# Kernel tuning notes

Measured on AMD Instinct MI355X. Metric: run time of the kernel, lower is better.

## Reference

```python
import jax, jax.numpy as jnp
import numpy as np

K = 2  # top-k experts per token


def setup_inputs() -> dict:
    key = jax.random.key(0)
    k1, k2 = jax.random.split(key)
    B, S, H, E = 4, 4096, 4096, 64
    x = jax.random.normal(k1, (B, S, H), dtype=jnp.float32)
    gate_w = jax.random.normal(k2, (E, H), dtype=jnp.float32) * (H ** -0.5)
    return {"x": x, "gate_w": gate_w}


def reference(x, gate_w):
    # logits = x @ gate_w.T : [B, S, E]
    logits = jnp.einsum("bsh,eh->bse", x, gate_w)
    scores = jax.nn.softmax(logits, axis=-1)
    topk_scores, topk_idx = jax.lax.top_k(scores, K)  # [B, S, K]
    aux_loss = scores.mean() * 0.0
    z_loss = jnp.mean(logits.astype(jnp.float32) ** 2)
    return topk_idx, topk_scores, aux_loss, z_loss
```

## Files before the change

kernel.cpp:

```cpp
#include <hip/hip_runtime.h>
#include <hip/hip_bf16.h>


typedef __bf16  bf16x8  __attribute__((ext_vector_type(8)));
typedef float   f32x16  __attribute__((ext_vector_type(16)));

#define BS_TOK 16384
#define H_DIM  4096
#define E_DIM  64
#define KSPLIT 4
#define KCHUNK (H_DIM / KSPLIT)
#define NPANEL (KCHUNK / 64)
#define WS_ZBUF_OFF (1536u << 10)
#define WS_LG_OFF   (2u << 20)

__device__ __forceinline__ void split3(float v, __bf16 &b0, __bf16 &b1, __bf16 &b2) {
    b0 = (__bf16)v;
    float r = v - (float)b0;
    b1 = (__bf16)r;
    float r2 = r - (float)b1;
    b2 = (__bf16)r2;
}

__device__ __forceinline__ void async_copy16(const float* gp, float* lp) {
    __builtin_amdgcn_global_load_lds(
        (const __attribute__((address_space(1))) void*)gp,
        (__attribute__((address_space(3))) void*)lp, 16, 0, 0);
}

__global__ void prep_w(const float* __restrict__ gw, bf16x8* __restrict__ wb) {
    int idx  = blockIdx.x * blockDim.x + threadIdx.x;
    int kb   = idx >> 7;
    int rem  = idx & 127;
    int nt   = rem >> 6;
    int lane = rem & 63;
    int n  = nt * 32 + (lane & 31);
    int kk = kb * 16 + ((lane >> 5) << 3);
    const float* p = gw + (size_t)n * H_DIM + kk;
    bf16x8 t0, t1, t2;
#pragma unroll
    for (int j = 0; j < 8; ++j) {
        __bf16 a, b, c;
        split3(p[j], a, b, c);
        t0[j] = a; t1[j] = b; t2[j] = c;
    }
    size_t fb = (size_t)(kb * 2 + nt) * 3;
    wb[(fb + 0) * 64 + lane] = t0;
    wb[(fb + 1) * 64 + lane] = t1;
    wb[(fb + 2) * 64 + lane] = t2;
}

__global__ __launch_bounds__(256, 4) void gemm_split(
        const float* __restrict__ x, const bf16x8* __restrict__ wb,
        float* __restrict__ lg) {
    __shared__ float lds[2 * 4096];

    int bid = blockIdx.x;
    int mt  = bid >> 2;
    int kc  = bid & 3;
    int tid = threadIdx.x;
    int w   = tid >> 6;
    int l   = tid & 63;
    int m0  = mt * 64;
    int rw  = (w & 1) * 32;
    int kh  = w >> 1;

    const float* gpan[4];
    int ldso[4];
    int s_slot = l & 15;
#pragma unroll
    for (int r = 0; r < 4; ++r) {
        int g = r * 16 + w * 4 + (l >> 4);
        int c = s_slot ^ (g & 15);
        gpan[r] = x + (size_t)(m0 + g) * H_DIM + kc * KCHUNK + c * 4;
        ldso[r] = (r * 16 + w * 4) * 64;
    }

    f32x16 acc0, acc1;
#pragma unroll
    for (int r = 0; r < 16; ++r) { acc0[r] = 0.f; acc1[r] = 0.f; }

#pragma unroll
    for (int r = 0; r < 4; ++r) async_copy16(gpan[r], &lds[ldso[r]]);

    int row  = rw + (l & 31);
    int half = l >> 5;
    int rsw  = row & 15;

    for (int p = 0; p < NPANEL; ++p) {
        __syncthreads();
        if (p + 1 < NPANEL) {
            int b = (p + 1) & 1;
#pragma unroll
            for (int r = 0; r < 4; ++r)
                async_copy16(gpan[r] + (p + 1) * 64, &lds[b * 4096 + ldso[r]]);
        }
        int bufo = (p & 1) * 4096;
#pragma unroll
        for (int ks2 = 0; ks2 < 2; ++ks2) {
            int ks     = kh * 2 + ks2;
            int ks_abs = kc * 64 + p * 4 + ks;
            int c0     = ks * 4 + half * 2;
            float4 xa = *(const float4*)&lds[bufo + row * 64 + ((c0 ^ rsw) << 2)];
            float4 xb = *(const float4*)&lds[bufo + row * 64 + (((c0 + 1) ^ rsw) << 2)];
            bf16x8 a0, a1, a2;
            float xs[8] = {xa.x, xa.y, xa.z, xa.w, xb.x, xb.y, xb.z, xb.w};
#pragma unroll
            for (int j = 0; j < 8; ++j) {
                __bf16 h0, h1, h2;
                split3(xs[j], h0, h1, h2);
                a0[j] = h0; a1[j] = h1; a2[j] = h2;
            }
            const bf16x8* wp = wb + (size_t)ks_abs * 6 * 64 + l;
            bf16x8 b0 = wp[0*64], b1 = wp[1*64], b2 = wp[2*64];
            bf16x8 b3 = wp[3*64], b4 = wp[4*64], b5 = wp[5*64];
            acc0 = __builtin_amdgcn_mfma_f32_32x32x16_bf16(a0, b0, acc0, 0, 0, 0);
            acc0 = __builtin_amdgcn_mfma_f32_32x32x16_bf16(a1, b0, acc0, 0, 0, 0);
            acc0 = __builtin_amdgcn_mfma_f32_32x32x16_bf16(a2, b0, acc0, 0, 0, 0);
            acc0 = __builtin_amdgcn_mfma_f32_32x32x16_bf16(a0, b1, acc0, 0, 0, 0);
            acc0 = __builtin_amdgcn_mfma_f32_32x32x16_bf16(a1, b1, acc0, 0, 0, 0);
            acc0 = __builtin_amdgcn_mfma_f32_32x32x16_bf16(a0, b2, acc0, 0, 0, 0);
            acc1 = __builtin_amdgcn_mfma_f32_32x32x16_bf16(a0, b3, acc1, 0, 0, 0);
            acc1 = __builtin_amdgcn_mfma_f32_32x32x16_bf16(a1, b3, acc1, 0, 0, 0);
            acc1 = __builtin_amdgcn_mfma_f32_32x32x16_bf16(a2, b3, acc1, 0, 0, 0);
            acc1 = __builtin_amdgcn_mfma_f32_32x32x16_bf16(a0, b4, acc1, 0, 0, 0);
            acc1 = __builtin_amdgcn_mfma_f32_32x32x16_bf16(a1, b4, acc1, 0, 0, 0);
            acc1 = __builtin_amdgcn_mfma_f32_32x32x16_bf16(a0, b5, acc1, 0, 0, 0);
        }
    }

    int col = l & 31;
    if (kh == 1) {
#pragma unroll
        for (int r = 0; r < 16; ++r) {
            int mm = rw + (r & 3) + ((r >> 2) << 3) + (half << 2);
            lds[mm * 64 + col]      = acc0[r];
            lds[mm * 64 + 32 + col] = acc1[r];
        }
    }
    __syncthreads();
    if (kh == 0) {
        size_t obase = (size_t)kc * BS_TOK * E_DIM + (size_t)m0 * E_DIM;
#pragma unroll
        for (int r = 0; r < 16; ++r) {
            int mm = rw + (r & 3) + ((r >> 2) << 3) + (half << 2);
            lg[obase + (size_t)mm * E_DIM + col]
                = acc0[r] + lds[mm * 64 + col];
            lg[obase + (size_t)mm * E_DIM + 32 + col]
                = acc1[r] + lds[mm * 64 + 32 + col];
        }
    }
}

__global__ __launch_bounds__(256) void epilogue(const float* __restrict__ lg,
                                                float* __restrict__ out,
                                                float* __restrict__ zbuf) {
    __shared__ float zsh[4];
    int lane = threadIdx.x & 63;
    int w    = threadIdx.x >> 6;
    int t    = blockIdx.x * 4 + w;

    float l = 0.f;
#pragma unroll
    for (int s = 0; s < KSPLIT; ++s)
        l += lg[((size_t)s * BS_TOK + t) * E_DIM + lane];

    float z = l * l;
#pragma unroll
    for (int off = 32; off; off >>= 1) z += __shfl_xor(z, off);
    if (lane == 0) zsh[w] = z;

    float m = l;
#pragma unroll
    for (int off = 32; off; off >>= 1) m = fmaxf(m, __shfl_xor(m, off));
    float e = expf(l - m);
    float d = e;
#pragma unroll
    for (int off = 32; off; off >>= 1) d += __shfl_xor(d, off);
    float sc = e / d;

    float s1 = sc; int i1 = lane;
#pragma unroll
    for (int off = 32; off; off >>= 1) {
        float os = __shfl_xor(s1, off); int oi = __shfl_xor(i1, off);
        if (os > s1 || (os == s1 && oi < i1)) { s1 = os; i1 = oi; }
    }
    float sm = (lane == i1) ? -1.0f : sc;
    float s2 = sm; int i2 = lane;
#pragma unroll
    for (int off = 32; off; off >>= 1) {
        float os = __shfl_xor(s2, off); int oi = __shfl_xor(i2, off);
        if (os > s2 || (os == s2 && oi < i2)) { s2 = os; i2 = oi; }
    }

    if (lane == 0) {
        out[2 * t]                  = (float)i1;
        out[2 * t + 1]              = (float)i2;
        out[2 * BS_TOK + 2 * t]     = s1;
        out[2 * BS_TOK + 2 * t + 1] = s2;
    }
    __syncthreads();
    if (threadIdx.x == 0)
        zbuf[blockIdx.x] = zsh[0] + zsh[1] + zsh[2] + zsh[3];
}

__global__ __launch_bounds__(256) void zreduce(const float* __restrict__ zbuf,
                                               float* __restrict__ out) {
    __shared__ float sh[4];
    int tid = threadIdx.x;
    float s = 0.f;
#pragma unroll
    for (int i = 0; i < 16; ++i) s += zbuf[tid + 256 * i];
#pragma unroll
    for (int off = 32; off; off >>= 1) s += __shfl_xor(s, off);
    if ((tid & 63) == 0) sh[tid >> 6] = s;
    __syncthreads();
    if (tid == 0) {
        out[4 * BS_TOK]     = 0.0f;
        out[4 * BS_TOK + 1] = (sh[0] + sh[1] + sh[2] + sh[3])
                              * (1.0f / (float)(BS_TOK * E_DIM));
    }
}

extern "C" void kernel_launch(void* const* d_in, const int* in_sizes, int n_in,
                              void* d_out, int out_size, void* d_ws, size_t ws_size,
                              hipStream_t stream) {
    const float* x  = (const float*)d_in[0];
    const float* gw = (const float*)d_in[1];
    float* out  = (float*)d_out;
    bf16x8* wb  = (bf16x8*)d_ws;
    float*  zbf = (float*)((char*)d_ws + WS_ZBUF_OFF);
    float*  lg  = (float*)((char*)d_ws + WS_LG_OFF);

    prep_w<<<128, 256, 0, stream>>>(gw, wb);
    gemm_split<<<(BS_TOK / 64) * KSPLIT, 256, 0, stream>>>(x, wb, lg);
    epilogue<<<BS_TOK / 4, 256, 0, stream>>>(lg, out, zbf);
    zreduce<<<1, 256, 0, stream>>>(zbf, out);
}
```

Baseline: 397.7 us.

## Fuse split-K router GEMM with softmax/top-k epilogue in one kernel

Replaces the split-K GEMM plus separate epilogue kernel with one fused kernel. Each block takes 32 tokens, and each wave owns a quarter of the hidden dimension with private double-buffered LDS panels. The per-wave partial logits are reduced in LDS, and softmax, top-2 and the z-loss partial are computed in place. This removes the global logits round-trip, one kernel launch, and the block-wide barriers inside the main loop, which become per-wave waitcnt. In exchange it uses 64KB of LDS per block and limits occupancy to 2 blocks per CU. The grid also shrinks to 512 blocks, which may cost latency hiding on the x stream.

```diff
diff --git a/kernel.cpp b/kernel.cpp
--- a/kernel.cpp
+++ b/kernel.cpp
@@ -8,11 +8,10 @@
 #define BS_TOK 16384
 #define H_DIM  4096
 #define E_DIM  64
-#define KSPLIT 4
-#define KCHUNK (H_DIM / KSPLIT)
-#define NPANEL (KCHUNK / 64)
+#define MT     32
+#define KWAVE  1024
+#define NPANEL 16
 #define WS_ZBUF_OFF (1536u << 10)
-#define WS_LG_OFF   (2u << 20)
 
 __device__ __forceinline__ void split3(float v, __bf16 &b0, __bf16 &b1, __bf16 &b2) {
     b0 = (__bf16)v;
@@ -50,30 +49,24 @@
     wb[(fb + 2) * 64 + lane] = t2;
 }
 
-__global__ __launch_bounds__(256, 4) void gemm_split(
+__global__ __launch_bounds__(256, 2) void fused_router(
         const float* __restrict__ x, const bf16x8* __restrict__ wb,
-        float* __restrict__ lg) {
-    __shared__ float lds[2 * 4096];
-
-    int bid = blockIdx.x;
-    int mt  = bid >> 2;
-    int kc  = bid & 3;
+        float* __restrict__ out, float* __restrict__ zbuf) {
+    __shared__ float lds[16384];
+    __shared__ float zsh[4];
+
     int tid = threadIdx.x;
     int w   = tid >> 6;
     int l   = tid & 63;
-    int m0  = mt * 64;
-    int rw  = (w & 1) * 32;
-    int kh  = w >> 1;
-
-    const float* gpan[4];
-    int ldso[4];
-    int s_slot = l & 15;
-#pragma unroll
-    for (int r = 0; r < 4; ++r) {
-        int g = r * 16 + w * 4 + (l >> 4);
-        int c = s_slot ^ (g & 15);
-        gpan[r] = x + (size_t)(m0 + g) * H_DIM + kc * KCHUNK + c * 4;
-        ldso[r] = (r * 16 + w * 4) * 64;
+    int m0  = blockIdx.x * MT;
+    float* sw = &lds[w * 4096];
+
+    const float* gp[8];
+#pragma unroll
+    for (int r = 0; r < 8; ++r) {
+        int g = 4 * r + (l >> 4);
+        int c = (l & 15) ^ (g & 15);
+        gp[r] = x + (size_t)(m0 + g) * H_DIM + w * KWAVE + c * 4;
     }
 
     f32x16 acc0, acc1;
@@ -81,28 +74,24 @@
     for (int r = 0; r < 16; ++r) { acc0[r] = 0.f; acc1[r] = 0.f; }
 
 #pragma unroll
-    for (int r = 0; r < 4; ++r) async_copy16(gpan[r], &lds[ldso[r]]);
-
-    int row  = rw + (l & 31);
-    int half = l >> 5;
-    int rsw  = row & 15;
+    for (int r = 0; r < 8; ++r) async_copy16(gp[r], sw + r * 256);
+
+    int row = l & 31, half = l >> 5, rsw = row & 15;
 
     for (int p = 0; p < NPANEL; ++p) {
-        __syncthreads();
+        __builtin_amdgcn_s_waitcnt(0x0F70);
         if (p + 1 < NPANEL) {
-            int b = (p + 1) & 1;
-#pragma unroll
-            for (int r = 0; r < 4; ++r)
-                async_copy16(gpan[r] + (p + 1) * 64, &lds[b * 4096 + ldso[r]]);
-        }
-        int bufo = (p & 1) * 4096;
-#pragma unroll
-        for (int ks2 = 0; ks2 < 2; ++ks2) {
-            int ks     = kh * 2 + ks2;
-            int ks_abs = kc * 64 + p * 4 + ks;
-            int c0     = ks * 4 + half * 2;
-            float4 xa = *(const float4*)&lds[bufo + row * 64 + ((c0 ^ rsw) << 2)];
-            float4 xb = *(const float4*)&lds[bufo + row * 64 + (((c0 + 1) ^ rsw) << 2)];
+            float* dst = sw + ((p + 1) & 1) * 2048;
+#pragma unroll
+            for (int r = 0; r < 8; ++r)
+                async_copy16(gp[r] + (p + 1) * 64, dst + r * 256);
+        }
+        const float* sb = sw + (p & 1) * 2048;
+#pragma unroll
+        for (int kk = 0; kk < 4; ++kk) {
+            int c0 = kk * 4 + half * 2;
+            float4 xa = *(const float4*)&sb[row * 64 + ((c0 ^ rsw) << 2)];
+            float4 xb = *(const float4*)&sb[row * 64 + (((c0 + 1) ^ rsw) << 2)];
             bf16x8 a0, a1, a2;
             float xs[8] = {xa.x, xa.y, xa.z, xa.w, xb.x, xb.y, xb.z, xb.w};
 #pragma unroll
@@ -111,6 +100,7 @@
                 split3(xs[j], h0, h1, h2);
                 a0[j] = h0; a1[j] = h1; a2[j] = h2;
             }
+            int ks_abs = w * 64 + p * 4 + kk;
             const bf16x8* wp = wb + (size_t)ks_abs * 6 * 64 + l;
             bf16x8 b0 = wp[0*64], b1 = wp[1*64], b2 = wp[2*64];
             bf16x8 b3 = wp[3*64], b4 = wp[4*64], b5 = wp[5*64];
@@ -129,78 +119,59 @@
         }
     }
 
+    __syncthreads();
     int col = l & 31;
-    if (kh == 1) {
-#pragma unroll
-        for (int r = 0; r < 16; ++r) {
-            int mm = rw + (r & 3) + ((r >> 2) << 3) + (half << 2);
-            lds[mm * 64 + col]      = acc0[r];
-            lds[mm * 64 + 32 + col] = acc1[r];
-        }
-    }
-    __syncthreads();
-    if (kh == 0) {
-        size_t obase = (size_t)kc * BS_TOK * E_DIM + (size_t)m0 * E_DIM;
-#pragma unroll
-        for (int r = 0; r < 16; ++r) {
-            int mm = rw + (r & 3) + ((r >> 2) << 3) + (half << 2);
-            lg[obase + (size_t)mm * E_DIM + col]
-                = acc0[r] + lds[mm * 64 + col];
-            lg[obase + (size_t)mm * E_DIM + 32 + col]
-                = acc1[r] + lds[mm * 64 + 32 + col];
-        }
-    }
-}
-
-__global__ __launch_bounds__(256) void epilogue(const float* __restrict__ lg,
-                                                float* __restrict__ out,
-                                                float* __restrict__ zbuf) {
-    __shared__ float zsh[4];
-    int lane = threadIdx.x & 63;
-    int w    = threadIdx.x >> 6;
-    int t    = blockIdx.x * 4 + w;
-
-    float l = 0.f;
-#pragma unroll
-    for (int s = 0; s < KSPLIT; ++s)
-        l += lg[((size_t)s * BS_TOK + t) * E_DIM + lane];
-
-    float z = l * l;
-#pragma unroll
-    for (int off = 32; off; off >>= 1) z += __shfl_xor(z, off);
-    if (lane == 0) zsh[w] = z;
-
-    float m = l;
-#pragma unroll
-    for (int off = 32; off; off >>= 1) m = fmaxf(m, __shfl_xor(m, off));
-    float e = expf(l - m);
-    float d = e;
-#pragma unroll
-    for (int off = 32; off; off >>= 1) d += __shfl_xor(d, off);
-    float sc = e / d;
-
-    float s1 = sc; int i1 = lane;
-#pragma unroll
-    for (int off = 32; off; off >>= 1) {
-        float os = __shfl_xor(s1, off); int oi = __shfl_xor(i1, off);
-        if (os > s1 || (os == s1 && oi < i1)) { s1 = os; i1 = oi; }
-    }
-    float sm = (lane == i1) ? -1.0f : sc;
-    float s2 = sm; int i2 = lane;
-#pragma unroll
-    for (int off = 32; off; off >>= 1) {
-        float os = __shfl_xor(s2, off); int oi = __shfl_xor(i2, off);
-        if (os > s2 || (os == s2 && oi < i2)) { s2 = os; i2 = oi; }
-    }
-
-    if (lane == 0) {
-        out[2 * t]                  = (float)i1;
-        out[2 * t + 1]              = (float)i2;
-        out[2 * BS_TOK + 2 * t]     = s1;
-        out[2 * BS_TOK + 2 * t + 1] = s2;
-    }
-    __syncthreads();
-    if (threadIdx.x == 0)
+#pragma unroll
+    for (int r = 0; r < 16; ++r) {
+        int mm = (r & 3) + ((r >> 2) << 3) + (half << 2);
+        lds[w * 2048 + mm * 64 + col]      = acc0[r];
+        lds[w * 2048 + mm * 64 + 32 + col] = acc1[r];
+    }
+    __syncthreads();
+
+    float zacc = 0.f;
+    for (int i = 0; i < 8; ++i) {
+        int tl = w * 8 + i;
+        float lg = lds[tl * 64 + l] + lds[2048 + tl * 64 + l]
+                 + lds[4096 + tl * 64 + l] + lds[6144 + tl * 64 + l];
+        zacc += lg * lg;
+
+        float m = lg;
+#pragma unroll
+        for (int off = 32; off; off >>= 1) m = fmaxf(m, __shfl_xor(m, off));
+        float e = expf(lg - m);
+        float d = e;
+#pragma unroll
+        for (int off = 32; off; off >>= 1) d += __shfl_xor(d, off);
+        float sc = e / d;
+
+        float s1 = sc; int i1 = l;
+#pragma unroll
+        for (int off = 32; off; off >>= 1) {
+            float os = __shfl_xor(s1, off); int oi = __shfl_xor(i1, off);
+            if (os > s1 || (os == s1 && oi < i1)) { s1 = os; i1 = oi; }
+        }
+        float sm = (l == i1) ? -1.0f : sc;
+        float s2 = sm; int i2 = l;
+#pragma unroll
+        for (int off = 32; off; off >>= 1) {
+            float os = __shfl_xor(s2, off); int oi = __shfl_xor(i2, off);
+            if (os > s2 || (os == s2 && oi < i2)) { s2 = os; i2 = oi; }
+        }
+
+        if (l == 0) {
+            int t = m0 + tl;
+            out[2 * t]                  = (float)i1;
+            out[2 * t + 1]              = (float)i2;
+            out[2 * BS_TOK + 2 * t]     = s1;
+            out[2 * BS_TOK + 2 * t + 1] = s2;
+        }
+    }
+#pragma unroll
+    for (int off = 32; off; off >>= 1) zacc += __shfl_xor(zacc, off);
+    if (l == 0) zsh[w] = zacc;
+    __syncthreads();
+    if (tid == 0)
         zbuf[blockIdx.x] = zsh[0] + zsh[1] + zsh[2] + zsh[3];
 }
 
@@ -208,9 +179,7 @@
                                                float* __restrict__ out) {
     __shared__ float sh[4];
     int tid = threadIdx.x;
-    float s = 0.f;
-#pragma unroll
-    for (int i = 0; i < 16; ++i) s += zbuf[tid + 256 * i];
+    float s = zbuf[tid] + zbuf[tid + 256];
 #pragma unroll
     for (int off = 32; off; off >>= 1) s += __shfl_xor(s, off);
     if ((tid & 63) == 0) sh[tid >> 6] = s;
@@ -230,10 +199,8 @@
     float* out  = (float*)d_out;
     bf16x8* wb  = (bf16x8*)d_ws;
     float*  zbf = (float*)((char*)d_ws + WS_ZBUF_OFF);
-    float*  lg  = (float*)((char*)d_ws + WS_LG_OFF);
 
     prep_w<<<128, 256, 0, stream>>>(gw, wb);
-    gemm_split<<<(BS_TOK / 64) * KSPLIT, 256, 0, stream>>>(x, wb, lg);
-    epilogue<<<BS_TOK / 4, 256, 0, stream>>>(lg, out, zbf);
+    fused_router<<<BS_TOK / MT, 256, 0, stream>>>(x, wb, out, zbf);
     zreduce<<<1, 256, 0, stream>>>(zbf, out);
 }
```

After: 410.4 us. 1.03x slower.
